# Kernel tuning notes

Hardware: AMD Instinct MI355X
Metric: run time of the kernel (lower is better)

## Reference

```python
import jax, jax.numpy as jnp
import numpy as np

B, S, D, H = 2, 4096, 512, 8
HD = D // H


def setup_inputs() -> dict:
    key = jax.random.key(0)
    ks = jax.random.split(key, 11)
    s = 1.0 / np.sqrt(D)
    return {
        "queries": jax.random.normal(ks[0], (B, S, D), jnp.float32),
        "keys": jax.random.normal(ks[1], (B, S, D), jnp.float32),
        "values": jax.random.normal(ks[2], (B, S, D), jnp.float32),
        "Wq": jax.random.normal(ks[3], (D, D), jnp.float32) * s,
        "bq": jnp.zeros((D,), jnp.float32),
        "Wk": jax.random.normal(ks[4], (D, D), jnp.float32) * s,
        "bk": jnp.zeros((D,), jnp.float32),
        "Wv": jax.random.normal(ks[5], (D, D), jnp.float32) * s,
        "bv": jnp.zeros((D,), jnp.float32),
        "Wo": jax.random.normal(ks[6], (D, D), jnp.float32) * s,
        "bo": jnp.zeros((D,), jnp.float32),
    }


def reference(queries, keys, values, Wq, bq, Wk, bk, Wv, bv, Wo, bo):
    b = queries.shape[0]
    # Linear projections (torch Linear: x @ W.T + b; here W stored as [in, out])
    q = (queries @ Wq + bq).reshape(b, -1, H, HD)   # [B, Sq, H, HD]
    k = (keys @ Wk + bk).reshape(b, -1, H, HD)       # [B, Sk, H, HD]
    v = (values @ Wv + bv).reshape(b, -1, H, HD)     # [B, Sk, H, HD]
    logits = jnp.einsum('bqhd,bkhd->bhqk', q, k) / jnp.sqrt(jnp.float32(HD))
    attn = jax.nn.softmax(logits, axis=-1)           # [B, H, Sq, Sk]  (dropout_rate=0 -> identity)
    ctx = jnp.einsum('bhqk,bkhd->bqhd', attn, v).reshape(b, -1, H * HD)
    return ctx @ Wo + bo
```

## Files before the change

kernel.cpp:

```cpp
#include <hip/hip_runtime.h>
#include <hip/hip_bf16.h>

constexpr int B_  = 2;
constexpr int S_  = 4096;
constexpr int D_  = 512;
constexpr int H_  = 8;
constexpr int HD_ = 64;
constexpr int M_  = B_ * S_;

typedef __attribute__((ext_vector_type(8))) short short8;
typedef __attribute__((ext_vector_type(4))) float floatx4;
typedef __attribute__((ext_vector_type(16))) float floatx16;

static __device__ __forceinline__ unsigned short f2bf(float f) {
    union { float f; unsigned u; } v; v.f = f;
    unsigned r = v.u + 0x7fffu + ((v.u >> 16) & 1u);
    return (unsigned short)(r >> 16);
}

static __device__ __forceinline__ unsigned pk2bf(float a, float b) {
#if __has_builtin(__builtin_amdgcn_cvt_pk_bf16_f32)
    typedef __attribute__((ext_vector_type(2))) __bf16 bf16x2_t;
    union { bf16x2_t v; unsigned u; } u;
    u.v = __builtin_amdgcn_cvt_pk_bf16_f32(a, b);
    return u.u;
#else
    return (unsigned)f2bf(a) | ((unsigned)f2bf(b) << 16);
#endif
}

static __device__ __forceinline__ void plane32swap(unsigned& x, unsigned& y) {
#if __has_builtin(__builtin_amdgcn_permlane32_swap)
    typedef __attribute__((ext_vector_type(2))) unsigned uint2v;
    uint2v r = __builtin_amdgcn_permlane32_swap(x, y, false, false);
    x = r[0]; y = r[1];
#else
    const bool hi = (threadIdx.x & 32) != 0;
    unsigned xs = __shfl_xor(x, 32), ys = __shfl_xor(y, 32);
    unsigned nx = hi ? ys : x;
    unsigned ny = hi ? y : xs;
    x = nx; y = ny;
#endif
}

#if __has_builtin(__builtin_amdgcn_exp2f)
#define EXP2(x) __builtin_amdgcn_exp2f(x)
#else
#define EXP2(x) exp2f(x)
#endif

#define QSCALE 0.18033688011110204f

static __device__ __forceinline__ void gl_lds16(const void* g, void* l) {
    typedef __attribute__((address_space(1))) const unsigned GU;
    typedef __attribute__((address_space(3))) unsigned LU;
    __builtin_amdgcn_global_load_lds((GU*)g, (LU*)l, 16, 0, 0);
}

__global__ __launch_bounds__(256) void xcast_kernel(
    const float* __restrict__ Xq, const float* __restrict__ Xk, const float* __restrict__ Xv,
    unsigned short* __restrict__ Y) {
    const int z = blockIdx.z;
    const float* X = z == 0 ? Xq : (z == 1 ? Xk : Xv);
    unsigned short* Yz = Y + (size_t)z * M_ * D_;
    const int n8 = M_ * D_ / 8;
    int i = blockIdx.x * 256 + threadIdx.x;
    const int stride = gridDim.x * 256;
    for (; i < n8; i += stride) {
        float4 a = *(const float4*)&X[(size_t)i * 8];
        float4 b = *(const float4*)&X[(size_t)i * 8 + 4];
        union { short8 s; unsigned u[4]; } p;
        p.u[0] = pk2bf(a.x, a.y); p.u[1] = pk2bf(a.z, a.w);
        p.u[2] = pk2bf(b.x, b.y); p.u[3] = pk2bf(b.z, b.w);
        *(short8*)&Yz[(size_t)i * 8] = p.s;
    }
}

__global__ __launch_bounds__(256) void wtrans_kernel(
    const float* __restrict__ Wq, const float* __restrict__ Wk,
    const float* __restrict__ Wv, const float* __restrict__ Wo,
    unsigned short* __restrict__ Tq, unsigned short* __restrict__ Tk,
    unsigned short* __restrict__ Tv, unsigned short* __restrict__ To) {
    const int z = blockIdx.z;
    const float* W = z == 0 ? Wq : (z == 1 ? Wk : (z == 2 ? Wv : Wo));
    unsigned short* Wt = z == 0 ? Tq : (z == 1 ? Tk : (z == 2 ? Tv : To));
    __shared__ float T[64][65];
    const int t = threadIdx.x;
    const int k0 = blockIdx.x * 64, n0 = blockIdx.y * 64;
#pragma unroll
    for (int i = 0; i < 4; ++i) {
        const int flat = t + 256 * i;
        const int kr = flat >> 4, nc = (flat & 15) * 4;
        float4 v = *(const float4*)&W[(size_t)(k0 + kr) * 512 + n0 + nc];
        T[kr][nc] = v.x; T[kr][nc + 1] = v.y; T[kr][nc + 2] = v.z; T[kr][nc + 3] = v.w;
    }
    __syncthreads();
#pragma unroll
    for (int i = 0; i < 4; ++i) {
        const int flat = t + 256 * i;
        const int nr = flat >> 4, kc = (flat & 15) * 4;
        ushort4 o4;
        o4.x = f2bf(T[kc][nr]);     o4.y = f2bf(T[kc + 1][nr]);
        o4.z = f2bf(T[kc + 2][nr]); o4.w = f2bf(T[kc + 3][nr]);
        *(ushort4*)&Wt[(size_t)(n0 + nr) * 512 + k0 + kc] = o4;
    }
}

template <int MODE>
__global__ __launch_bounds__(256, 3) void gemm_kernel(
    const unsigned short* __restrict__ Ab,
    const unsigned short* __restrict__ Wt,
    const float* __restrict__ b0, const float* __restrict__ b1, const float* __restrict__ b2,
    unsigned short* __restrict__ o0, unsigned short* __restrict__ o1,
    unsigned short* __restrict__ o2, float* __restrict__ of) {
    __shared__ unsigned short As[128 * 64];
    __shared__ unsigned short Bs[128 * 64];

    const int tid  = threadIdx.x;
    const int w    = tid >> 6;
    const int lane = tid & 63;
    const int n0   = blockIdx.x * 128;
    const int m0   = blockIdx.y * 128;
    const int lm   = lane & 15;
    const int lq   = lane >> 4;
    const int wm   = (w >> 1) * 64;
    const int wn   = (w & 1) * 64;

    const int z = MODE == 0 ? (n0 >> 9) : 0;
    const unsigned short* A = MODE == 0 ? Ab + (size_t)z * M_ * D_ : Ab;

    const int srow = lane >> 3;
    const int sch  = lane & 7;
    const int ca   = (sch ^ (srow & 7)) * 8;

    floatx4 acc[4][4];
#pragma unroll
    for (int i = 0; i < 4; ++i)
#pragma unroll
        for (int j = 0; j < 4; ++j) acc[i][j] = (floatx4)0.0f;

    for (int kb = 0; kb < 8; ++kb) {
        const int k0 = kb * 64;
        __syncthreads();
#pragma unroll
        for (int it = 0; it < 4; ++it) {
            const int r8 = w * 32 + it * 8;
            gl_lds16(&A [(size_t)(m0 + r8 + srow) * 512 + k0 + ca], &As[r8 * 64]);
            gl_lds16(&Wt[(size_t)(n0 + r8 + srow) * 512 + k0 + ca], &Bs[r8 * 64]);
        }
        __syncthreads();

        short8 af[2][4], bf[2][4];
#pragma unroll
        for (int ks = 0; ks < 2; ++ks)
#pragma unroll
            for (int i = 0; i < 4; ++i) {
                const int cc = ((ks * 4 + lq) ^ (lm & 7)) * 8;
                af[ks][i] = *(const short8*)&As[(wm + i * 16 + lm) * 64 + cc];
                bf[ks][i] = *(const short8*)&Bs[(wn + i * 16 + lm) * 64 + cc];
            }
#pragma unroll
        for (int ks = 0; ks < 2; ++ks)
#pragma unroll
            for (int mi = 0; mi < 4; ++mi)
#pragma unroll
                for (int ni = 0; ni < 4; ++ni)
                    acc[mi][ni] = __builtin_amdgcn_mfma_f32_16x16x32_bf16(
                        af[ks][mi], bf[ks][ni], acc[mi][ni], 0, 0, 0);
    }

    const float* bias = MODE == 0 ? (z == 0 ? b0 : (z == 1 ? b1 : b2)) : b0;
    const float scale = (MODE == 0 && z == 0) ? QSCALE : 1.0f;
    const int nl0 = n0 & 511;

    float bias_n[4];
#pragma unroll
    for (int ni = 0; ni < 4; ++ni) bias_n[ni] = bias[nl0 + wn + ni * 16 + lm];

#pragma unroll
    for (int mi = 0; mi < 4; ++mi) {
#pragma unroll
        for (int ni = 0; ni < 4; ++ni) {
            if (MODE == 1) {
                const int gn = n0 + wn + ni * 16 + lm;
#pragma unroll
                for (int r = 0; r < 4; ++r) {
                    const int gm = m0 + wm + mi * 16 + lq * 4 + r;
                    of[(size_t)gm * 512 + gn] = acc[mi][ni][r] + bias_n[ni];
                }
            } else {
                const int gnl = nl0 + wn + ni * 16 + lm;
                const int h = gnl >> 6, hd = gnl & 63;
                if (z == 2) {
                    const int gm = m0 + wm + mi * 16 + lq * 4;
                    const int b = gm >> 12, s = gm & 4095;
                    union { ushort4 s4; uint2 u; } o4;
                    o4.u.x = pk2bf(acc[mi][ni][0] + bias_n[ni], acc[mi][ni][1] + bias_n[ni]);
                    o4.u.y = pk2bf(acc[mi][ni][2] + bias_n[ni], acc[mi][ni][3] + bias_n[ni]);
                    *(ushort4*)&o2[(((size_t)(b * 8 + h)) * 64 + hd) * 4096 + s] = o4.s4;
                } else {
                    unsigned short* out = z == 0 ? o0 : o1;
#pragma unroll
                    for (int r = 0; r < 4; ++r) {
                        const int gm = m0 + wm + mi * 16 + lq * 4 + r;
                        const int b = gm >> 12, s = gm & 4095;
                        const float vv = (acc[mi][ni][r] + bias_n[ni]) * scale;
                        out[(((size_t)(b * 8 + h)) * 4096 + s) * 64 + hd] = f2bf(vv);
                    }
                }
            }
        }
    }
}

__global__ __launch_bounds__(256, 2) void flash_kernel(
    const unsigned short* __restrict__ Q, const unsigned short* __restrict__ K,
    const unsigned short* __restrict__ Vt, unsigned short* __restrict__ ctx) {
    __shared__ unsigned short Ks[64 * 64];
    __shared__ unsigned short Vs[64 * 64];

    const int tid = threadIdx.x;
    const int w   = tid >> 6;
    const int l   = tid & 63;
    const int lo  = l & 31;
    const int hi  = l >> 5;
    const int lo7 = lo & 7;
    const int q0  = blockIdx.x * 128;
    const int bh  = blockIdx.y;
    const int qw  = q0 + w * 32;

    const size_t base = (size_t)bh * S_ * HD_;
    const unsigned short* Qg = Q + base;
    const unsigned short* Kg = K + base;
    const unsigned short* Vg = Vt + base;

    short8 qf[4];
#pragma unroll
    for (int ds = 0; ds < 4; ++ds)
        qf[ds] = *(const short8*)&Qg[(size_t)(qw + lo) * 64 + ds * 16 + hi * 8];

    short8 ones;
#pragma unroll
    for (int j = 0; j < 8; ++j) ones[j] = (short)0x3F80;

    floatx16 o[2];
    o[0] = (floatx16)0.0f; o[1] = (floatx16)0.0f;
    floatx16 lacc = (floatx16)0.0f;

    const int sr  = tid >> 3, sch = tid & 7;
    const int swz = (sch ^ (sr & 7)) * 8;
    const int sw0 = sr * 64 + swz;
    const int sw1 = (sr + 32) * 64 + swz;

    short8 kr0, kr1, vr0, vr1;
    kr0 = *(const short8*)&Kg[(size_t)sr * 64 + sch * 8];
    kr1 = *(const short8*)&Kg[(size_t)(sr + 32) * 64 + sch * 8];
    vr0 = *(const short8*)&Vg[(size_t)sr * S_ + sch * 8];
    vr1 = *(const short8*)&Vg[(size_t)(sr + 32) * S_ + sch * 8];

    for (int kt = 0; kt < 64; ++kt) {
        __syncthreads();
        *(short8*)&Ks[sw0] = kr0;
        *(short8*)&Ks[sw1] = kr1;
        *(short8*)&Vs[sw0] = vr0;
        *(short8*)&Vs[sw1] = vr1;
        __syncthreads();
        if (kt < 63) {
            const int t1 = (kt + 1) * 64;
            kr0 = *(const short8*)&Kg[(size_t)(t1 + sr) * 64 + sch * 8];
            kr1 = *(const short8*)&Kg[(size_t)(t1 + sr + 32) * 64 + sch * 8];
            vr0 = *(const short8*)&Vg[(size_t)sr * S_ + t1 + sch * 8];
            vr1 = *(const short8*)&Vg[(size_t)(sr + 32) * S_ + t1 + sch * 8];
        }

        short8 kf[2][4];
#pragma unroll
        for (int g = 0; g < 2; ++g)
#pragma unroll
            for (int ds = 0; ds < 4; ++ds)
                kf[g][ds] = *(const short8*)&Ks[(g * 32 + lo) * 64 +
                                                (((ds * 2 + hi) ^ lo7) * 8)];
        floatx16 s[2];
        s[0] = (floatx16)0.0f; s[1] = (floatx16)0.0f;
#pragma unroll
        for (int g = 0; g < 2; ++g)
#pragma unroll
            for (int ds = 0; ds < 4; ++ds)
                s[g] = __builtin_amdgcn_mfma_f32_32x32x16_bf16(
                    kf[g][ds], qf[ds], s[g], 0, 0, 0);

        floatx16 p[2];
#pragma unroll
        for (int g = 0; g < 2; ++g)
#pragma unroll
            for (int r = 0; r < 16; ++r) p[g][r] = EXP2(s[g][r]);

        short8 pa[4];
#pragma unroll
        for (int ks = 0; ks < 4; ++ks) {
            const int g = ks >> 1, kk = (ks & 1) * 8;
            unsigned wa = pk2bf(p[g][kk + 0], p[g][kk + 1]);
            unsigned wb = pk2bf(p[g][kk + 2], p[g][kk + 3]);
            unsigned wc = pk2bf(p[g][kk + 4], p[g][kk + 5]);
            unsigned wd = pk2bf(p[g][kk + 6], p[g][kk + 7]);
            plane32swap(wa, wc);
            plane32swap(wb, wd);
            union { short8 s8; unsigned u[4]; } pk_;
            pk_.u[0] = wa; pk_.u[1] = wb; pk_.u[2] = wc; pk_.u[3] = wd;
            pa[ks] = pk_.s8;
        }

        short8 vf[2][4];
#pragma unroll
        for (int onn = 0; onn < 2; ++onn)
#pragma unroll
            for (int ks = 0; ks < 4; ++ks)
                vf[onn][ks] = *(const short8*)&Vs[(onn * 32 + lo) * 64 +
                                                  (((ks * 2 + hi) ^ lo7) * 8)];
#pragma unroll
        for (int ks = 0; ks < 4; ++ks) {
            lacc = __builtin_amdgcn_mfma_f32_32x32x16_bf16(pa[ks], ones, lacc, 0, 0, 0);
            o[0] = __builtin_amdgcn_mfma_f32_32x32x16_bf16(pa[ks], vf[0][ks], o[0], 0, 0, 0);
            o[1] = __builtin_amdgcn_mfma_f32_32x32x16_bf16(pa[ks], vf[1][ks], o[1], 0, 0, 0);
        }
    }

    const int b = bh >> 3, h = bh & 7;
#pragma unroll
    for (int r = 0; r < 16; ++r) {
        const float inv = 1.0f / lacc[r];
        const int q = qw + (r & 3) + 8 * (r >> 2) + 4 * hi;
        unsigned short* cp = &ctx[((size_t)(b * S_ + q)) * 512 + h * 64 + lo];
        cp[0]  = f2bf(o[0][r] * inv);
        cp[32] = f2bf(o[1][r] * inv);
    }
}

extern "C" void kernel_launch(void* const* d_in, const int* in_sizes, int n_in,
                              void* d_out, int out_size, void* d_ws, size_t ws_size,
                              hipStream_t stream) {
    const float* queries = (const float*)d_in[0];
    const float* keys    = (const float*)d_in[1];
    const float* values  = (const float*)d_in[2];
    const float* Wq = (const float*)d_in[3];
    const float* bq = (const float*)d_in[4];
    const float* Wk = (const float*)d_in[5];
    const float* bk = (const float*)d_in[6];
    const float* Wv = (const float*)d_in[7];
    const float* bv = (const float*)d_in[8];
    const float* Wo = (const float*)d_in[9];
    const float* bo = (const float*)d_in[10];

    unsigned short* xb    = (unsigned short*)d_ws;
    unsigned short* wsctx = xb;
    unsigned short* wsq   = xb   + (size_t)3 * M_ * D_;
    unsigned short* wsk   = wsq  + (size_t)M_ * D_;
    unsigned short* wsvt  = wsk  + (size_t)M_ * D_;
    unsigned short* wtq   = wsvt + (size_t)M_ * D_;
    unsigned short* wtk   = wtq  + (size_t)D_ * D_;
    unsigned short* wtv   = wtk  + (size_t)D_ * D_;
    unsigned short* wto   = wtv  + (size_t)D_ * D_;

    xcast_kernel<<<dim3(1024, 1, 3), dim3(256), 0, stream>>>(queries, keys, values, xb);
    wtrans_kernel<<<dim3(8, 8, 4), dim3(256), 0, stream>>>(
        Wq, Wk, Wv, Wo, wtq, wtk, wtv, wto);

    gemm_kernel<0><<<dim3(12, 64), dim3(256), 0, stream>>>(
        xb, wtq, bq, bk, bv, wsq, wsk, wsvt, nullptr);

    flash_kernel<<<dim3(S_ / 128, B_ * H_), dim3(256), 0, stream>>>(wsq, wsk, wsvt, wsctx);

    gemm_kernel<1><<<dim3(4, 64), dim3(256), 0, stream>>>(
        wsctx, wto, bo, nullptr, nullptr, nullptr, nullptr, nullptr, (float*)d_out);
}
```

Baseline: 239.7 us.

## Split flash attention over key dimension, double-buffer LDS tiles, add reduce kernel

Flash attention now optionally splits the key range in two (grid z=2). Each half writes unnormalized fp32 partial outputs and row sums to workspace, and a new reduce kernel combines them into bf16 ctx. K/V tiles are double-buffered in shared memory with a single barrier per iteration, s_setprio is raised around the MFMA blocks, and launch bounds go to 4 blocks per CU. This aims to raise occupancy and parallelism, since the base grid of 512 blocks is small for the CU count. The cost is extra fp32 partial traffic plus an additional kernel launch. The split path runs only if the workspace is at least 92 MB.

```diff
diff --git a/kernel.cpp b/kernel.cpp
--- a/kernel.cpp
+++ b/kernel.cpp
@@ -213,11 +213,14 @@
     }
 }
 
-__global__ __launch_bounds__(256, 2) void flash_kernel(
+template <int KSPLIT>
+__global__ __launch_bounds__(256, 4) void flash_kernel(
     const unsigned short* __restrict__ Q, const unsigned short* __restrict__ K,
-    const unsigned short* __restrict__ Vt, unsigned short* __restrict__ ctx) {
-    __shared__ unsigned short Ks[64 * 64];
-    __shared__ unsigned short Vs[64 * 64];
+    const unsigned short* __restrict__ Vt, unsigned short* __restrict__ ctx,
+    float* __restrict__ Op, float* __restrict__ Lp) {
+    constexpr int NT = 64 / KSPLIT;
+    __shared__ unsigned short Ks[2][64 * 64];
+    __shared__ unsigned short Vs[2][64 * 64];
 
     const int tid = threadIdx.x;
     const int w   = tid >> 6;
@@ -227,6 +230,8 @@
     const int lo7 = lo & 7;
     const int q0  = blockIdx.x * 128;
     const int bh  = blockIdx.y;
+    const int kz  = (KSPLIT == 1) ? 0 : blockIdx.z;
+    const int kb0 = kz * NT * 64;
     const int qw  = q0 + w * 32;
 
     const size_t base = (size_t)bh * S_ * HD_;
@@ -253,41 +258,60 @@
     const int sw1 = (sr + 32) * 64 + swz;
 
     short8 kr0, kr1, vr0, vr1;
-    kr0 = *(const short8*)&Kg[(size_t)sr * 64 + sch * 8];
-    kr1 = *(const short8*)&Kg[(size_t)(sr + 32) * 64 + sch * 8];
-    vr0 = *(const short8*)&Vg[(size_t)sr * S_ + sch * 8];
-    vr1 = *(const short8*)&Vg[(size_t)(sr + 32) * S_ + sch * 8];
-
-    for (int kt = 0; kt < 64; ++kt) {
+    auto LOADT = [&](int t) {
+        const int krow = kb0 + t * 64;
+        kr0 = *(const short8*)&Kg[(size_t)(krow + sr) * 64 + sch * 8];
+        kr1 = *(const short8*)&Kg[(size_t)(krow + sr + 32) * 64 + sch * 8];
+        vr0 = *(const short8*)&Vg[(size_t)sr * S_ + krow + sch * 8];
+        vr1 = *(const short8*)&Vg[(size_t)(sr + 32) * S_ + krow + sch * 8];
+    };
+
+    LOADT(0);
+    *(short8*)&Ks[0][sw0] = kr0;
+    *(short8*)&Ks[0][sw1] = kr1;
+    *(short8*)&Vs[0][sw0] = vr0;
+    *(short8*)&Vs[0][sw1] = vr1;
+    if (NT > 1) LOADT(1);
+
+    for (int kt = 0; kt < NT; ++kt) {
+        const int cb = kt & 1;
         __syncthreads();
-        *(short8*)&Ks[sw0] = kr0;
-        *(short8*)&Ks[sw1] = kr1;
-        *(short8*)&Vs[sw0] = vr0;
-        *(short8*)&Vs[sw1] = vr1;
-        __syncthreads();
-        if (kt < 63) {
-            const int t1 = (kt + 1) * 64;
-            kr0 = *(const short8*)&Kg[(size_t)(t1 + sr) * 64 + sch * 8];
-            kr1 = *(const short8*)&Kg[(size_t)(t1 + sr + 32) * 64 + sch * 8];
-            vr0 = *(const short8*)&Vg[(size_t)sr * S_ + t1 + sch * 8];
-            vr1 = *(const short8*)&Vg[(size_t)(sr + 32) * S_ + t1 + sch * 8];
-        }
+        if (kt + 1 < NT) {
+            *(short8*)&Ks[cb ^ 1][sw0] = kr0;
+            *(short8*)&Ks[cb ^ 1][sw1] = kr1;
+            *(short8*)&Vs[cb ^ 1][sw0] = vr0;
+            *(short8*)&Vs[cb ^ 1][sw1] = vr1;
+        }
+        if (kt + 2 < NT) LOADT(kt + 2);
+
+        const unsigned short* Kc = Ks[cb];
+        const unsigned short* Vc = Vs[cb];
 
         short8 kf[2][4];
 #pragma unroll
         for (int g = 0; g < 2; ++g)
 #pragma unroll
             for (int ds = 0; ds < 4; ++ds)
-                kf[g][ds] = *(const short8*)&Ks[(g * 32 + lo) * 64 +
+                kf[g][ds] = *(const short8*)&Kc[(g * 32 + lo) * 64 +
                                                 (((ds * 2 + hi) ^ lo7) * 8)];
+        short8 vf[2][4];
+#pragma unroll
+        for (int onn = 0; onn < 2; ++onn)
+#pragma unroll
+            for (int ks = 0; ks < 4; ++ks)
+                vf[onn][ks] = *(const short8*)&Vc[(onn * 32 + lo) * 64 +
+                                                  (((ks * 2 + hi) ^ lo7) * 8)];
+
         floatx16 s[2];
         s[0] = (floatx16)0.0f; s[1] = (floatx16)0.0f;
+        __builtin_amdgcn_s_setprio(1);
 #pragma unroll
         for (int g = 0; g < 2; ++g)
 #pragma unroll
             for (int ds = 0; ds < 4; ++ds)
                 s[g] = __builtin_amdgcn_mfma_f32_32x32x16_bf16(
                     kf[g][ds], qf[ds], s[g], 0, 0, 0);
+        __builtin_amdgcn_s_setprio(0);
 
         floatx16 p[2];
 #pragma unroll
@@ -310,29 +334,58 @@
             pa[ks] = pk_.s8;
         }
 
-        short8 vf[2][4];
-#pragma unroll
-        for (int onn = 0; onn < 2; ++onn)
-#pragma unroll
-            for (int ks = 0; ks < 4; ++ks)
-                vf[onn][ks] = *(const short8*)&Vs[(onn * 32 + lo) * 64 +
-                                                  (((ks * 2 + hi) ^ lo7) * 8)];
+        __builtin_amdgcn_s_setprio(1);
 #pragma unroll
         for (int ks = 0; ks < 4; ++ks) {
             lacc = __builtin_amdgcn_mfma_f32_32x32x16_bf16(pa[ks], ones, lacc, 0, 0, 0);
             o[0] = __builtin_amdgcn_mfma_f32_32x32x16_bf16(pa[ks], vf[0][ks], o[0], 0, 0, 0);
             o[1] = __builtin_amdgcn_mfma_f32_32x32x16_bf16(pa[ks], vf[1][ks], o[1], 0, 0, 0);
         }
-    }
-
-    const int b = bh >> 3, h = bh & 7;
-#pragma unroll
-    for (int r = 0; r < 16; ++r) {
-        const float inv = 1.0f / lacc[r];
-        const int q = qw + (r & 3) + 8 * (r >> 2) + 4 * hi;
-        unsigned short* cp = &ctx[((size_t)(b * S_ + q)) * 512 + h * 64 + lo];
-        cp[0]  = f2bf(o[0][r] * inv);
-        cp[32] = f2bf(o[1][r] * inv);
+        __builtin_amdgcn_s_setprio(0);
+    }
+
+    if (KSPLIT == 1) {
+        const int b = bh >> 3, h = bh & 7;
+#pragma unroll
+        for (int r = 0; r < 16; ++r) {
+            const float inv = 1.0f / lacc[r];
+            const int q = qw + (r & 3) + 8 * (r >> 2) + 4 * hi;
+            unsigned short* cp = &ctx[((size_t)(b * S_ + q)) * 512 + h * 64 + lo];
+            cp[0]  = f2bf(o[0][r] * inv);
+            cp[32] = f2bf(o[1][r] * inv);
+        }
+    } else {
+        float* Ob = Op + ((size_t)(kz * 16 + bh) * S_) * 64;
+        float* Lb = Lp + (size_t)(kz * 16 + bh) * S_;
+#pragma unroll
+        for (int r = 0; r < 16; ++r) {
+            const int q = qw + (r & 3) + 8 * (r >> 2) + 4 * hi;
+            Ob[(size_t)q * 64 + lo]      = o[0][r];
+            Ob[(size_t)q * 64 + lo + 32] = o[1][r];
+            if (lo == 0) Lb[q] = lacc[r];
+        }
+    }
+}
+
+__global__ __launch_bounds__(256) void reduce_kernel(
+    const float* __restrict__ Op, const float* __restrict__ Lp,
+    unsigned short* __restrict__ ctx) {
+    constexpr int ROWS = 16 * S_;
+    constexpr int SPLIT_F = ROWS * 64;
+    const int total = ROWS * 16;
+    int i = blockIdx.x * 256 + threadIdx.x;
+    const int stride = gridDim.x * 256;
+    for (; i < total; i += stride) {
+        const int r = i >> 4, c4 = (i & 15) * 4;
+        float4 a = *(const float4*)&Op[(size_t)r * 64 + c4];
+        float4 c = *(const float4*)&Op[(size_t)r * 64 + c4 + SPLIT_F];
+        const float inv = 1.0f / (Lp[r] + Lp[r + ROWS]);
+        const int bh = r >> 12, q = r & 4095;
+        const int b = bh >> 3, h = bh & 7;
+        union { ushort4 s; uint2 u; } o4;
+        o4.u.x = pk2bf((a.x + c.x) * inv, (a.y + c.y) * inv);
+        o4.u.y = pk2bf((a.z + c.z) * inv, (a.w + c.w) * inv);
+        *(ushort4*)&ctx[((size_t)(b * S_ + q)) * 512 + h * 64 + c4] = o4.s;
     }
 }
 
@@ -361,6 +414,11 @@
     unsigned short* wtv   = wtk  + (size_t)D_ * D_;
     unsigned short* wto   = wtv  + (size_t)D_ * D_;
 
+    const size_t op_off = 52428800ULL;
+    float* Op = (float*)((char*)d_ws + op_off);
+    float* Lp = (float*)((char*)d_ws + op_off + 33554432ULL);
+    const bool split2 = ws_size >= (size_t)92 * 1024 * 1024;
+
     xcast_kernel<<<dim3(1024, 1, 3), dim3(256), 0, stream>>>(queries, keys, values, xb);
     wtrans_kernel<<<dim3(8, 8, 4), dim3(256), 0, stream>>>(
         Wq, Wk, Wv, Wo, wtq, wtk, wtv, wto);
@@ -368,7 +426,14 @@
     gemm_kernel<0><<<dim3(12, 64), dim3(256), 0, stream>>>(
         xb, wtq, bq, bk, bv, wsq, wsk, wsvt, nullptr);
 
-    flash_kernel<<<dim3(S_ / 128, B_ * H_), dim3(256), 0, stream>>>(wsq, wsk, wsvt, wsctx);
+    if (split2) {
+        flash_kernel<2><<<dim3(S_ / 128, B_ * H_, 2), dim3(256), 0, stream>>>(
+            wsq, wsk, wsvt, nullptr, Op, Lp);
+        reduce_kernel<<<dim3(2048), dim3(256), 0, stream>>>(Op, Lp, wsctx);
+    } else {
+        flash_kernel<1><<<dim3(S_ / 128, B_ * H_, 1), dim3(256), 0, stream>>>(
+            wsq, wsk, wsvt, wsctx, nullptr, nullptr);
+    }
 
     gemm_kernel<1><<<dim3(4, 64), dim3(256), 0, stream>>>(
         wsctx, wto, bo, nullptr, nullptr, nullptr, nullptr, nullptr, (float*)d_out);
```

After: 632.2 us. +163.7%, slower.

## Fuse input fp32-to-bf16 cast into QKV GEMM and double-buffer flash K/V via LDS DMA

Applied to the files above, without the earlier changes.

Removes the separate xcast kernel. The QKV projection GEMM now loads fp32 activations directly, converts them to bf16 in registers and writes them to swizzled LDS, which saves a full write and re-read of the bf16 copy. The flash attention kernel switches from register staging to double-buffered global_load_lds for K/V tiles, removing one barrier per iteration. It also raises wave priority around the MFMA blocks. The tradeoff is that GEMM A loads now go through registers at twice the bytes, and the GEMM iterations are not pipelined.

```diff
diff --git a/kernel.cpp b/kernel.cpp
--- a/kernel.cpp
+++ b/kernel.cpp
@@ -57,25 +57,6 @@
     __builtin_amdgcn_global_load_lds((GU*)g, (LU*)l, 16, 0, 0);
 }
 
-__global__ __launch_bounds__(256) void xcast_kernel(
-    const float* __restrict__ Xq, const float* __restrict__ Xk, const float* __restrict__ Xv,
-    unsigned short* __restrict__ Y) {
-    const int z = blockIdx.z;
-    const float* X = z == 0 ? Xq : (z == 1 ? Xk : Xv);
-    unsigned short* Yz = Y + (size_t)z * M_ * D_;
-    const int n8 = M_ * D_ / 8;
-    int i = blockIdx.x * 256 + threadIdx.x;
-    const int stride = gridDim.x * 256;
-    for (; i < n8; i += stride) {
-        float4 a = *(const float4*)&X[(size_t)i * 8];
-        float4 b = *(const float4*)&X[(size_t)i * 8 + 4];
-        union { short8 s; unsigned u[4]; } p;
-        p.u[0] = pk2bf(a.x, a.y); p.u[1] = pk2bf(a.z, a.w);
-        p.u[2] = pk2bf(b.x, b.y); p.u[3] = pk2bf(b.z, b.w);
-        *(short8*)&Yz[(size_t)i * 8] = p.s;
-    }
-}
-
 __global__ __launch_bounds__(256) void wtrans_kernel(
     const float* __restrict__ Wq, const float* __restrict__ Wk,
     const float* __restrict__ Wv, const float* __restrict__ Wo,
@@ -108,6 +89,8 @@
 
 template <int MODE>
 __global__ __launch_bounds__(256, 3) void gemm_kernel(
+    const float* __restrict__ Xq, const float* __restrict__ Xk,
+    const float* __restrict__ Xv,
     const unsigned short* __restrict__ Ab,
     const unsigned short* __restrict__ Wt,
     const float* __restrict__ b0, const float* __restrict__ b1, const float* __restrict__ b2,
@@ -127,7 +110,7 @@
     const int wn   = (w & 1) * 64;
 
     const int z = MODE == 0 ? (n0 >> 9) : 0;
-    const unsigned short* A = MODE == 0 ? Ab + (size_t)z * M_ * D_ : Ab;
+    const float* Xz = MODE == 0 ? (z == 0 ? Xq : (z == 1 ? Xk : Xv)) : nullptr;
 
     const int srow = lane >> 3;
     const int sch  = lane & 7;
@@ -142,11 +125,31 @@
     for (int kb = 0; kb < 8; ++kb) {
         const int k0 = kb * 64;
         __syncthreads();
-#pragma unroll
-        for (int it = 0; it < 4; ++it) {
-            const int r8 = w * 32 + it * 8;
-            gl_lds16(&A [(size_t)(m0 + r8 + srow) * 512 + k0 + ca], &As[r8 * 64]);
-            gl_lds16(&Wt[(size_t)(n0 + r8 + srow) * 512 + k0 + ca], &Bs[r8 * 64]);
+        if (MODE == 0) {
+            float4 fa[4], fb[4];
+#pragma unroll
+            for (int it = 0; it < 4; ++it) {
+                const int r8 = w * 32 + it * 8;
+                const float* src = &Xz[(size_t)(m0 + r8 + srow) * 512 + k0 + ca];
+                fa[it] = *(const float4*)src;
+                fb[it] = *(const float4*)(src + 4);
+                gl_lds16(&Wt[(size_t)(n0 + r8 + srow) * 512 + k0 + ca], &Bs[r8 * 64]);
+            }
+#pragma unroll
+            for (int it = 0; it < 4; ++it) {
+                const int r8 = w * 32 + it * 8;
+                union { short8 s; unsigned u[4]; } p;
+                p.u[0] = pk2bf(fa[it].x, fa[it].y); p.u[1] = pk2bf(fa[it].z, fa[it].w);
+                p.u[2] = pk2bf(fb[it].x, fb[it].y); p.u[3] = pk2bf(fb[it].z, fb[it].w);
+                *(short8*)&As[(r8 + srow) * 64 + sch * 8] = p.s;
+            }
+        } else {
+#pragma unroll
+            for (int it = 0; it < 4; ++it) {
+                const int r8 = w * 32 + it * 8;
+                gl_lds16(&Ab[(size_t)(m0 + r8 + srow) * 512 + k0 + ca], &As[r8 * 64]);
+                gl_lds16(&Wt[(size_t)(n0 + r8 + srow) * 512 + k0 + ca], &Bs[r8 * 64]);
+            }
         }
         __syncthreads();
 
@@ -216,8 +219,9 @@
 __global__ __launch_bounds__(256, 2) void flash_kernel(
     const unsigned short* __restrict__ Q, const unsigned short* __restrict__ K,
     const unsigned short* __restrict__ Vt, unsigned short* __restrict__ ctx) {
-    __shared__ unsigned short Ks[64 * 64];
-    __shared__ unsigned short Vs[64 * 64];
+    constexpr int NT = 64;
+    __shared__ unsigned short Ks[2][64 * 64];
+    __shared__ unsigned short Vs[2][64 * 64];
 
     const int tid = threadIdx.x;
     const int w   = tid >> 6;
@@ -248,61 +252,57 @@
     floatx16 lacc = (floatx16)0.0f;
 
     const int sr  = tid >> 3, sch = tid & 7;
-    const int swz = (sch ^ (sr & 7)) * 8;
-    const int sw0 = sr * 64 + swz;
-    const int sw1 = (sr + 32) * 64 + swz;
-
-    short8 kr0, kr1, vr0, vr1;
-    kr0 = *(const short8*)&Kg[(size_t)sr * 64 + sch * 8];
-    kr1 = *(const short8*)&Kg[(size_t)(sr + 32) * 64 + sch * 8];
-    vr0 = *(const short8*)&Vg[(size_t)sr * S_ + sch * 8];
-    vr1 = *(const short8*)&Vg[(size_t)(sr + 32) * S_ + sch * 8];
-
-    for (int kt = 0; kt < 64; ++kt) {
+    const int cs  = (sch ^ (sr & 7)) * 8;
+
+    auto STAGE = [&](int t, int bb) {
+        const int krow = t * 64;
+        gl_lds16(&Kg[(size_t)(krow + sr) * 64 + cs],      &Ks[bb][(w * 8) * 64]);
+        gl_lds16(&Kg[(size_t)(krow + sr + 32) * 64 + cs], &Ks[bb][(w * 8 + 32) * 64]);
+        gl_lds16(&Vg[(size_t)sr * S_ + krow + cs],        &Vs[bb][(w * 8) * 64]);
+        gl_lds16(&Vg[(size_t)(sr + 32) * S_ + krow + cs], &Vs[bb][(w * 8 + 32) * 64]);
+    };
+
+    STAGE(0, 0);
+
+    for (int kt = 0; kt < NT; ++kt) {
+        const int cb = kt & 1;
         __syncthreads();
-        *(short8*)&Ks[sw0] = kr0;
-        *(short8*)&Ks[sw1] = kr1;
-        *(short8*)&Vs[sw0] = vr0;
-        *(short8*)&Vs[sw1] = vr1;
-        __syncthreads();
-        if (kt < 63) {
-            const int t1 = (kt + 1) * 64;
-            kr0 = *(const short8*)&Kg[(size_t)(t1 + sr) * 64 + sch * 8];
-            kr1 = *(const short8*)&Kg[(size_t)(t1 + sr + 32) * 64 + sch * 8];
-            vr0 = *(const short8*)&Vg[(size_t)sr * S_ + t1 + sch * 8];
-            vr1 = *(const short8*)&Vg[(size_t)(sr + 32) * S_ + t1 + sch * 8];
-        }
+        if (kt + 1 < NT) STAGE(kt + 1, cb ^ 1);
+
+        const unsigned short* Kc = Ks[cb];
+        const unsigned short* Vc = Vs[cb];
 
         short8 kf[2][4];
 #pragma unroll
         for (int g = 0; g < 2; ++g)
 #pragma unroll
             for (int ds = 0; ds < 4; ++ds)
-                kf[g][ds] = *(const short8*)&Ks[(g * 32 + lo) * 64 +
+                kf[g][ds] = *(const short8*)&Kc[(g * 32 + lo) * 64 +
                                                 (((ds * 2 + hi) ^ lo7) * 8)];
         floatx16 s[2];
         s[0] = (floatx16)0.0f; s[1] = (floatx16)0.0f;
+        __builtin_amdgcn_s_setprio(1);
 #pragma unroll
         for (int g = 0; g < 2; ++g)
 #pragma unroll
             for (int ds = 0; ds < 4; ++ds)
                 s[g] = __builtin_amdgcn_mfma_f32_32x32x16_bf16(
                     kf[g][ds], qf[ds], s[g], 0, 0, 0);
-
-        floatx16 p[2];
+        __builtin_amdgcn_s_setprio(0);
+
 #pragma unroll
         for (int g = 0; g < 2; ++g)
 #pragma unroll
-            for (int r = 0; r < 16; ++r) p[g][r] = EXP2(s[g][r]);
+            for (int r = 0; r < 16; ++r) s[g][r] = EXP2(s[g][r]);
 
         short8 pa[4];
 #pragma unroll
         for (int ks = 0; ks < 4; ++ks) {
             const int g = ks >> 1, kk = (ks & 1) * 8;
-            unsigned wa = pk2bf(p[g][kk + 0], p[g][kk + 1]);
-            unsigned wb = pk2bf(p[g][kk + 2], p[g][kk + 3]);
-            unsigned wc = pk2bf(p[g][kk + 4], p[g][kk + 5]);
-            unsigned wd = pk2bf(p[g][kk + 6], p[g][kk + 7]);
+            unsigned wa = pk2bf(s[g][kk + 0], s[g][kk + 1]);
+            unsigned wb = pk2bf(s[g][kk + 2], s[g][kk + 3]);
+            unsigned wc = pk2bf(s[g][kk + 4], s[g][kk + 5]);
+            unsigned wd = pk2bf(s[g][kk + 6], s[g][kk + 7]);
             plane32swap(wa, wc);
             plane32swap(wb, wd);
             union { short8 s8; unsigned u[4]; } pk_;
@@ -315,14 +315,16 @@
         for (int onn = 0; onn < 2; ++onn)
 #pragma unroll
             for (int ks = 0; ks < 4; ++ks)
-                vf[onn][ks] = *(const short8*)&Vs[(onn * 32 + lo) * 64 +
+                vf[onn][ks] = *(const short8*)&Vc[(onn * 32 + lo) * 64 +
                                                   (((ks * 2 + hi) ^ lo7) * 8)];
+        __builtin_amdgcn_s_setprio(1);
 #pragma unroll
         for (int ks = 0; ks < 4; ++ks) {
             lacc = __builtin_amdgcn_mfma_f32_32x32x16_bf16(pa[ks], ones, lacc, 0, 0, 0);
             o[0] = __builtin_amdgcn_mfma_f32_32x32x16_bf16(pa[ks], vf[0][ks], o[0], 0, 0, 0);
             o[1] = __builtin_amdgcn_mfma_f32_32x32x16_bf16(pa[ks], vf[1][ks], o[1], 0, 0, 0);
         }
+        __builtin_amdgcn_s_setprio(0);
     }
 
     const int b = bh >> 3, h = bh & 7;
@@ -351,25 +353,28 @@
     const float* Wo = (const float*)d_in[9];
     const float* bo = (const float*)d_in[10];
 
-    unsigned short* xb    = (unsigned short*)d_ws;
-    unsigned short* wsctx = xb;
-    unsigned short* wsq   = xb   + (size_t)3 * M_ * D_;
-    unsigned short* wsk   = wsq  + (size_t)M_ * D_;
-    unsigned short* wsvt  = wsk  + (size_t)M_ * D_;
-    unsigned short* wtq   = wsvt + (size_t)M_ * D_;
-    unsigned short* wtk   = wtq  + (size_t)D_ * D_;
-    unsigned short* wtv   = wtk  + (size_t)D_ * D_;
-    unsigned short* wto   = wtv  + (size_t)D_ * D_;
-
-    xcast_kernel<<<dim3(1024, 1, 3), dim3(256), 0, stream>>>(queries, keys, values, xb);
+    unsigned short* wsctx = (unsigned short*)d_ws;
+    unsigned short* wsq   = wsctx + (size_t)M_ * D_;
+    unsigned short* wsk   = wsq   + (size_t)M_ * D_;
+    unsigned short* wsvt  = wsk   + (size_t)M_ * D_;
+    unsigned short* wtq   = wsvt  + (size_t)M_ * D_;
+    unsigned short* wtk   = wtq   + (size_t)D_ * D_;
+    unsigned short* wtv   = wtk   + (size_t)D_ * D_;
+    unsigned short* wto   = wtv   + (size_t)D_ * D_;
+
     wtrans_kernel<<<dim3(8, 8, 4), dim3(256), 0, stream>>>(
         Wq, Wk, Wv, Wo, wtq, wtk, wtv, wto);
 
     gemm_kernel<0><<<dim3(12, 64), dim3(256), 0, stream>>>(
-        xb, wtq, bq, bk, bv, wsq, wsk, wsvt, nullptr);
+        queries, keys, values, nullptr, wtq,
+        bq, bk, bv, wsq, wsk, wsvt, nullptr);
 
     flash_kernel<<<dim3(S_ / 128, B_ * H_), dim3(256), 0, stream>>>(wsq, wsk, wsvt, wsctx);
 
     gemm_kernel<1><<<dim3(4, 64), dim3(256), 0, stream>>>(
-        wsctx, wto, bo, nullptr, nullptr, nullptr, nullptr, nullptr, (float*)d_out);
-}
+        (const float*)nullptr, (const float*)nullptr, (const float*)nullptr,
+        wsctx, wto,
+        bo, (const float*)nullptr, (const float*)nullptr,
+        (unsigned short*)nullptr, (unsigned short*)nullptr, (unsigned short*)nullptr,
+        (float*)d_out);
+}
```

Result: slower. 259.7 us (+8.3%).

## Double-buffer K/V tiles in LDS, process two tiles per barrier, raise MFMA priority

Applied to the files above, without the earlier changes.

The flash attention loop now keeps two LDS buffers, each holding two 64-key K/V tiles, and issues the global loads two iterations ahead. Each pass has one barrier instead of two and computes over two tiles per pass. MFMA sections are wrapped in s_setprio so matrix work is favoured over other waves. In exchange LDS use rises from 16 KB to 64 KB per block and prefetch registers double, which may cut occupancy below the two-blocks-per-CU target.

```diff
diff --git a/kernel.cpp b/kernel.cpp
--- a/kernel.cpp
+++ b/kernel.cpp
@@ -216,8 +216,9 @@
 __global__ __launch_bounds__(256, 2) void flash_kernel(
     const unsigned short* __restrict__ Q, const unsigned short* __restrict__ K,
     const unsigned short* __restrict__ Vt, unsigned short* __restrict__ ctx) {
-    __shared__ unsigned short Ks[64 * 64];
-    __shared__ unsigned short Vs[64 * 64];
+    constexpr int NO = 32;
+    __shared__ unsigned short Ks[2][2][64 * 64];
+    __shared__ unsigned short Vs[2][2][64 * 64];
 
     const int tid = threadIdx.x;
     const int w   = tid >> 6;
@@ -252,76 +253,95 @@
     const int sw0 = sr * 64 + swz;
     const int sw1 = (sr + 32) * 64 + swz;
 
-    short8 kr0, kr1, vr0, vr1;
-    kr0 = *(const short8*)&Kg[(size_t)sr * 64 + sch * 8];
-    kr1 = *(const short8*)&Kg[(size_t)(sr + 32) * 64 + sch * 8];
-    vr0 = *(const short8*)&Vg[(size_t)sr * S_ + sch * 8];
-    vr1 = *(const short8*)&Vg[(size_t)(sr + 32) * S_ + sch * 8];
-
-    for (int kt = 0; kt < 64; ++kt) {
+    short8 kr[2][2], vr[2][2];
+    auto LOADT2 = [&](int t2) {
+#pragma unroll
+        for (int j = 0; j < 2; ++j) {
+            const int krow = (t2 * 2 + j) * 64;
+            kr[j][0] = *(const short8*)&Kg[(size_t)(krow + sr) * 64 + sch * 8];
+            kr[j][1] = *(const short8*)&Kg[(size_t)(krow + sr + 32) * 64 + sch * 8];
+            vr[j][0] = *(const short8*)&Vg[(size_t)sr * S_ + krow + sch * 8];
+            vr[j][1] = *(const short8*)&Vg[(size_t)(sr + 32) * S_ + krow + sch * 8];
+        }
+    };
+    auto WRITE2 = [&](int bb) {
+#pragma unroll
+        for (int j = 0; j < 2; ++j) {
+            *(short8*)&Ks[bb][j][sw0] = kr[j][0];
+            *(short8*)&Ks[bb][j][sw1] = kr[j][1];
+            *(short8*)&Vs[bb][j][sw0] = vr[j][0];
+            *(short8*)&Vs[bb][j][sw1] = vr[j][1];
+        }
+    };
+
+    LOADT2(0);
+    WRITE2(0);
+    LOADT2(1);
+
+    for (int it = 0; it < NO; ++it) {
+        const int cb = it & 1;
         __syncthreads();
-        *(short8*)&Ks[sw0] = kr0;
-        *(short8*)&Ks[sw1] = kr1;
-        *(short8*)&Vs[sw0] = vr0;
-        *(short8*)&Vs[sw1] = vr1;
-        __syncthreads();
-        if (kt < 63) {
-            const int t1 = (kt + 1) * 64;
-            kr0 = *(const short8*)&Kg[(size_t)(t1 + sr) * 64 + sch * 8];
-            kr1 = *(const short8*)&Kg[(size_t)(t1 + sr + 32) * 64 + sch * 8];
-            vr0 = *(const short8*)&Vg[(size_t)sr * S_ + t1 + sch * 8];
-            vr1 = *(const short8*)&Vg[(size_t)(sr + 32) * S_ + t1 + sch * 8];
-        }
-
-        short8 kf[2][4];
-#pragma unroll
-        for (int g = 0; g < 2; ++g)
-#pragma unroll
-            for (int ds = 0; ds < 4; ++ds)
-                kf[g][ds] = *(const short8*)&Ks[(g * 32 + lo) * 64 +
-                                                (((ds * 2 + hi) ^ lo7) * 8)];
-        floatx16 s[2];
-        s[0] = (floatx16)0.0f; s[1] = (floatx16)0.0f;
-#pragma unroll
-        for (int g = 0; g < 2; ++g)
-#pragma unroll
-            for (int ds = 0; ds < 4; ++ds)
-                s[g] = __builtin_amdgcn_mfma_f32_32x32x16_bf16(
-                    kf[g][ds], qf[ds], s[g], 0, 0, 0);
-
-        floatx16 p[2];
-#pragma unroll
-        for (int g = 0; g < 2; ++g)
-#pragma unroll
-            for (int r = 0; r < 16; ++r) p[g][r] = EXP2(s[g][r]);
-
-        short8 pa[4];
-#pragma unroll
-        for (int ks = 0; ks < 4; ++ks) {
-            const int g = ks >> 1, kk = (ks & 1) * 8;
-            unsigned wa = pk2bf(p[g][kk + 0], p[g][kk + 1]);
-            unsigned wb = pk2bf(p[g][kk + 2], p[g][kk + 3]);
-            unsigned wc = pk2bf(p[g][kk + 4], p[g][kk + 5]);
-            unsigned wd = pk2bf(p[g][kk + 6], p[g][kk + 7]);
-            plane32swap(wa, wc);
-            plane32swap(wb, wd);
-            union { short8 s8; unsigned u[4]; } pk_;
-            pk_.u[0] = wa; pk_.u[1] = wb; pk_.u[2] = wc; pk_.u[3] = wd;
-            pa[ks] = pk_.s8;
-        }
-
-        short8 vf[2][4];
-#pragma unroll
-        for (int onn = 0; onn < 2; ++onn)
-#pragma unroll
-            for (int ks = 0; ks < 4; ++ks)
-                vf[onn][ks] = *(const short8*)&Vs[(onn * 32 + lo) * 64 +
-                                                  (((ks * 2 + hi) ^ lo7) * 8)];
-#pragma unroll
-        for (int ks = 0; ks < 4; ++ks) {
-            lacc = __builtin_amdgcn_mfma_f32_32x32x16_bf16(pa[ks], ones, lacc, 0, 0, 0);
-            o[0] = __builtin_amdgcn_mfma_f32_32x32x16_bf16(pa[ks], vf[0][ks], o[0], 0, 0, 0);
-            o[1] = __builtin_amdgcn_mfma_f32_32x32x16_bf16(pa[ks], vf[1][ks], o[1], 0, 0, 0);
+        if (it + 1 < NO) WRITE2(cb ^ 1);
+        if (it + 2 < NO) LOADT2(it + 2);
+
+#pragma unroll
+        for (int j = 0; j < 2; ++j) {
+            const unsigned short* Kc = Ks[cb][j];
+            const unsigned short* Vc = Vs[cb][j];
+
+            short8 kf[2][4];
+#pragma unroll
+            for (int g = 0; g < 2; ++g)
+#pragma unroll
+                for (int ds = 0; ds < 4; ++ds)
+                    kf[g][ds] = *(const short8*)&Kc[(g * 32 + lo) * 64 +
+                                                    (((ds * 2 + hi) ^ lo7) * 8)];
+            floatx16 s[2];
+            s[0] = (floatx16)0.0f; s[1] = (floatx16)0.0f;
+            __builtin_amdgcn_s_setprio(1);
+#pragma unroll
+            for (int g = 0; g < 2; ++g)
+#pragma unroll
+                for (int ds = 0; ds < 4; ++ds)
+                    s[g] = __builtin_amdgcn_mfma_f32_32x32x16_bf16(
+                        kf[g][ds], qf[ds], s[g], 0, 0, 0);
+            __builtin_amdgcn_s_setprio(0);
+
+#pragma unroll
+            for (int g = 0; g < 2; ++g)
+#pragma unroll
+                for (int r = 0; r < 16; ++r) s[g][r] = EXP2(s[g][r]);
+
+            short8 pa[4];
+#pragma unroll
+            for (int ks = 0; ks < 4; ++ks) {
+                const int g = ks >> 1, kk = (ks & 1) * 8;
+                unsigned wa = pk2bf(s[g][kk + 0], s[g][kk + 1]);
+                unsigned wb = pk2bf(s[g][kk + 2], s[g][kk + 3]);
+                unsigned wc = pk2bf(s[g][kk + 4], s[g][kk + 5]);
+                unsigned wd = pk2bf(s[g][kk + 6], s[g][kk + 7]);
+                plane32swap(wa, wc);
+                plane32swap(wb, wd);
+                union { short8 s8; unsigned u[4]; } pk_;
+                pk_.u[0] = wa; pk_.u[1] = wb; pk_.u[2] = wc; pk_.u[3] = wd;
+                pa[ks] = pk_.s8;
+            }
+
+            short8 vf[2][4];
+#pragma unroll
+            for (int onn = 0; onn < 2; ++onn)
+#pragma unroll
+                for (int ks = 0; ks < 4; ++ks)
+                    vf[onn][ks] = *(const short8*)&Vc[(onn * 32 + lo) * 64 +
+                                                      (((ks * 2 + hi) ^ lo7) * 8)];
+            __builtin_amdgcn_s_setprio(1);
+#pragma unroll
+            for (int ks = 0; ks < 4; ++ks) {
+                lacc = __builtin_amdgcn_mfma_f32_32x32x16_bf16(pa[ks], ones, lacc, 0, 0, 0);
+                o[0] = __builtin_amdgcn_mfma_f32_32x32x16_bf16(pa[ks], vf[0][ks], o[0], 0, 0, 0);
+                o[1] = __builtin_amdgcn_mfma_f32_32x32x16_bf16(pa[ks], vf[1][ks], o[1], 0, 0, 0);
+            }
+            __builtin_amdgcn_s_setprio(0);
         }
     }
 
```

Result: no change. 244.1 us (+1.8%).
